# Performance work log

Hardware: AMD Instinct MI355X
Metric: run time of the kernel (lower is better)

The kernel has to match this reference:

```python
import jax, jax.numpy as jnp
import numpy as np

B_SZ, SEQ, D_MODEL, D_STATE, EXPAND = 2, 1024, 1024, 16, 2
D_INNER = D_MODEL * EXPAND


def setup_inputs() -> dict:
    key = jax.random.key(0)
    ks = jax.random.split(key, 11)
    f32 = jnp.float32
    x = jax.random.normal(ks[0], (B_SZ, SEQ, D_MODEL), f32)
    # nn.Linear-style params (weight stored as [out, in], applied as x @ W.T + b)
    s_in = 1.0 / np.sqrt(D_MODEL)
    W_in = jax.random.uniform(ks[1], (2 * D_INNER, D_MODEL), f32, -s_in, s_in)
    b_in = jax.random.uniform(ks[2], (2 * D_INNER,), f32, -s_in, s_in)
    W_gate = jax.random.uniform(ks[3], (D_INNER, D_MODEL), f32, -s_in, s_in)
    b_gate = jax.random.uniform(ks[4], (D_INNER,), f32, -s_in, s_in)
    s_out = 1.0 / np.sqrt(D_INNER)
    W_out = jax.random.uniform(ks[5], (D_MODEL, D_INNER), f32, -s_out, s_out)
    b_out = jax.random.uniform(ks[6], (D_MODEL,), f32, -s_out, s_out)
    A_log = jax.random.uniform(ks[7], (D_INNER, D_STATE), f32, -3.0, -1.0)
    B_mat = 0.02 * jax.random.normal(ks[8], (D_INNER, D_STATE), f32)
    C_mat = 0.02 * jax.random.normal(ks[9], (D_INNER, D_STATE), f32)
    D_vec = 0.02 * jax.random.normal(ks[10], (D_INNER,), f32)
    return {"x": x, "W_in": W_in, "b_in": b_in, "W_gate": W_gate,
            "b_gate": b_gate, "W_out": W_out, "b_out": b_out,
            "A_log": A_log, "B_mat": B_mat, "C_mat": C_mat, "D_vec": D_vec}


def _selective_scan(x, delta, A_log, B_mat, C_mat, D_vec):
    # x, delta: [B, S, d_inner]
    A = -jnp.exp(A_log)            # [d_inner, d_state]
    c0 = C_mat[0]                  # [d_state]; torch code's [:,0,:,0] reads only C row 0

    def step(h, inp):
        x_t, d_t = inp             # each [B, d_inner]
        h = h * jnp.exp(A * d_t[..., None]) + (x_t * d_t)[..., None] * B_mat
        y_t = h @ c0               # [B, d_inner]
        return h, y_t

    h0 = jnp.zeros((x.shape[0], A.shape[0], A.shape[1]), x.dtype)
    xs = (jnp.moveaxis(x, 1, 0), jnp.moveaxis(delta, 1, 0))  # time-major
    _, ys = jax.lax.scan(step, h0, xs)                       # ys: [S, B, d_inner]
    y = jnp.moveaxis(ys, 0, 1)
    return y + x * D_vec


def reference(x, W_in, b_in, W_gate, b_gate, W_out, b_out, A_log, B_mat, C_mat, D_vec):
    gate = jax.nn.sigmoid(x @ W_gate.T + b_gate)            # [B,S,d_inner]
    proj = x @ W_in.T + b_in                                # [B,S,2*d_inner]
    x_proj, delta_proj = jnp.split(proj, 2, axis=-1)
    delta = jax.nn.relu(delta_proj)
    ss = _selective_scan(x_proj, delta, A_log, B_mat, C_mat, D_vec)
    return (gate * ss) @ W_out.T + b_out                    # [B,S,d_model]
```

## Files before the change

kernel.cpp:

```cpp
#include <hip/hip_runtime.h>
#include <hip/hip_bf16.h>


#define LOG2E 1.4426950408889634f

typedef float floatx4 __attribute__((ext_vector_type(4)));
typedef short short8 __attribute__((ext_vector_type(8)));

__device__ __forceinline__ float fexp2(float x) { return __builtin_amdgcn_exp2f(x); }
__device__ __forceinline__ unsigned short f2bf(float f) {
    unsigned int u = __float_as_uint(f);
    u = (u + 0x7fffu + ((u >> 16) & 1u)) >> 16;
    return (unsigned short)u;
}
__device__ __forceinline__ float bf2f(unsigned short h) {
    return __uint_as_float(((unsigned int)h) << 16);
}

#define GLDS16(gp, lp) __builtin_amdgcn_global_load_lds(                      \
    (const __attribute__((address_space(1))) void*)(gp),                      \
    (__attribute__((address_space(3))) void*)(lp), 16, 0, 0)

__global__ __launch_bounds__(256) void cast_to_bf16(
    const float* __restrict__ x, const float* __restrict__ wg,
    const float* __restrict__ wi, const float* __restrict__ wo,
    unsigned short* __restrict__ ox, unsigned short* __restrict__ owg,
    unsigned short* __restrict__ owi, unsigned short* __restrict__ owo)
{
    const size_t e = ((size_t)blockIdx.x * 256 + threadIdx.x) * 4;
    const float* src; unsigned short* dst; size_t off;
    if (e < 2097152)      { src = x;  dst = ox;  off = e; }
    else if (e < 4194304) { src = wg; dst = owg; off = e - 2097152; }
    else if (e < 8388608) { src = wi; dst = owi; off = e - 4194304; }
    else                  { src = wo; dst = owo; off = e - 8388608; }
    float4 v = *(const float4*)(src + off);
    *(ushort4*)(dst + off) = make_ushort4(f2bf(v.x), f2bf(v.y), f2bf(v.z), f2bf(v.w));
}

template <int MODE, int MI>
__global__ __launch_bounds__(256, 2) void gemm_mfma(
    const unsigned short* __restrict__ A,
    const unsigned short* __restrict__ W0,
    const unsigned short* __restrict__ W1,
    const float* __restrict__ bias0, const float* __restrict__ bias1,
    unsigned short* __restrict__ gate,
    float* __restrict__ xproj, float* __restrict__ delta,
    float* __restrict__ outp, int K)
{
    constexpr int BM = MI * 32;
    constexpr int ROWA = BM / 32;
    __shared__ short As[BM * 64];
    __shared__ short Bs[128 * 64];

    const int tid = threadIdx.x;
    const int l = tid & 63, w = tid >> 6;
    const int mbase = blockIdx.y * BM;

    const unsigned short* Wp; const float* bias; int nbase; bool isGate = false;
    if (MODE == 3) {
        const int bx = blockIdx.x;
        if (bx < 16) { Wp = W0; bias = bias0; nbase = bx * 128; isGate = true; }
        else         { Wp = W1; bias = bias1; nbase = (bx - 16) * 128; }
    } else { Wp = W0; bias = bias0; nbase = blockIdx.x * 128; }

    const int rl = l >> 3;
    const int cs = (l & 7) ^ rl;
    size_t aoff[ROWA], boff[4];
    #pragma unroll
    for (int j = 0; j < ROWA; ++j)
        aoff[j] = (size_t)(mbase + (w * ROWA + j) * 8 + rl) * K + cs * 8;
    #pragma unroll
    for (int j = 0; j < 4; ++j)
        boff[j] = (size_t)(nbase + (w * 4 + j) * 8 + rl) * K + cs * 8;

    const int wm = (w >> 1) * (MI * 16), wn = (w & 1) * 64;
    floatx4 acc[MI][4] = {};

    for (int k0 = 0; k0 < K; k0 += 64) {
        __syncthreads();
        #pragma unroll
        for (int j = 0; j < ROWA; ++j)
            GLDS16(A + aoff[j] + k0, &As[(w * ROWA + j) * 512]);
        #pragma unroll
        for (int j = 0; j < 4; ++j)
            GLDS16(Wp + boff[j] + k0, &Bs[(w * 4 + j) * 512]);
        __syncthreads();

        #pragma unroll
        for (int kk = 0; kk < 2; ++kk) {
            short8 af[MI], bfr[4];
            #pragma unroll
            for (int i = 0; i < MI; ++i) {
                const int row = wm + i * 16 + (l & 15);
                af[i] = *(const short8*)&As[row * 64 + (((kk * 4 + (l >> 4)) ^ (row & 7)) << 3)];
            }
            #pragma unroll
            for (int j = 0; j < 4; ++j) {
                const int row = wn + j * 16 + (l & 15);
                bfr[j] = *(const short8*)&Bs[row * 64 + (((kk * 4 + (l >> 4)) ^ (row & 7)) << 3)];
            }
            #pragma unroll
            for (int i = 0; i < MI; ++i)
                #pragma unroll
                for (int j = 0; j < 4; ++j)
                    acc[i][j] = __builtin_amdgcn_mfma_f32_16x16x32_bf16(af[i], bfr[j], acc[i][j], 0, 0, 0);
        }
    }

    const int crow0 = wm + (l >> 4) * 4;
    const int ccol = wn + (l & 15);
    #pragma unroll
    for (int j = 0; j < 4; ++j) {
        const int n = nbase + ccol + j * 16;
        const float bb = bias[n];
        #pragma unroll
        for (int i = 0; i < MI; ++i) {
            const int mr = mbase + crow0 + i * 16;
            #pragma unroll
            for (int r = 0; r < 4; ++r) {
                const float v = acc[i][j][r] + bb;
                const int m = mr + r;
                if (MODE == 3) {
                    if (isGate) {
                        const float s = 1.0f / (1.0f + fexp2(-v * LOG2E));
                        gate[(size_t)m * 2048 + n] = f2bf(s);
                    } else if (n < 2048) {
                        xproj[(size_t)m * 2048 + n] = v;
                    } else {
                        delta[(size_t)m * 2048 + (n - 2048)] = fmaxf(v, 0.0f);
                    }
                } else {
                    outp[(size_t)m * 1024 + n] = v;
                }
            }
        }
    }
}

constexpr int NC = 32, CL = 32;

__global__ __launch_bounds__(256) void scan_phaseA(
    const float* __restrict__ xp, const float* __restrict__ dl,
    const float* __restrict__ A_log, const float* __restrict__ B_mat,
    float* __restrict__ Q, float* __restrict__ sumdt)
{
    const int ch = blockIdx.x * 256 + threadIdx.x;
    const int c = blockIdx.y;
    const int d = ch & 2047, b = ch >> 11;
    float Ac[16], Bv[16], h[16];
    #pragma unroll
    for (int s = 0; s < 16; ++s) {
        Ac[s] = -fexp2(A_log[d * 16 + s] * LOG2E) * LOG2E;
        Bv[s] = B_mat[d * 16 + s];
        h[s] = 0.0f;
    }
    float sd = 0.0f;
    size_t idx = ((size_t)b * 1024 + (size_t)c * CL) * 2048 + d;
    for (int t = 0; t < CL; ++t, idx += 2048) {
        const float xt = xp[idx], dt = dl[idx];
        sd += dt;
        const float xdt = xt * dt;
        #pragma unroll
        for (int s = 0; s < 16; ++s)
            h[s] = fmaf(h[s], fexp2(Ac[s] * dt), xdt * Bv[s]);
    }
    float* q = Q + ((size_t)ch * NC + c) * 16;
    #pragma unroll
    for (int s = 0; s < 16; ++s) q[s] = h[s];
    sumdt[ch * NC + c] = sd;
}

__global__ __launch_bounds__(256) void scan_phaseB(
    const float* __restrict__ A_log, const float* __restrict__ Q,
    const float* __restrict__ sumdt, float* __restrict__ hst)
{
    const int s = threadIdx.x & 15;
    const int ch = blockIdx.x * 16 + (threadIdx.x >> 4);
    const int d = ch & 2047;
    const float Ac = -fexp2(A_log[d * 16 + s] * LOG2E) * LOG2E;
    float h = 0.0f;
    const float* q = Q + (size_t)ch * NC * 16 + s;
    const float* sd = sumdt + ch * NC;
    float* hs = hst + (size_t)ch * NC * 16 + s;
    for (int c = 0; c < NC; ++c) {
        hs[c * 16] = h;
        h = fmaf(h, fexp2(Ac * sd[c]), q[c * 16]);
    }
}

__global__ __launch_bounds__(256) void scan_phaseC(
    const float* __restrict__ xp, const float* __restrict__ dl,
    const float* __restrict__ A_log, const float* __restrict__ B_mat,
    const float* __restrict__ C_mat, const float* __restrict__ D_vec,
    const unsigned short* __restrict__ gate, const float* __restrict__ hst,
    unsigned short* __restrict__ z)
{
    const int ch = blockIdx.x * 256 + threadIdx.x;
    const int c = blockIdx.y;
    const int d = ch & 2047, b = ch >> 11;
    float Ac[16], Bv[16], Cv[16], h[16];
    #pragma unroll
    for (int s = 0; s < 16; ++s) {
        Ac[s] = -fexp2(A_log[d * 16 + s] * LOG2E) * LOG2E;
        Bv[s] = B_mat[d * 16 + s];
        Cv[s] = C_mat[s];
        h[s] = hst[((size_t)ch * NC + c) * 16 + s];
    }
    const float Dv = D_vec[d];
    size_t idx = ((size_t)b * 1024 + (size_t)c * CL) * 2048 + d;
    for (int t = 0; t < CL; ++t, idx += 2048) {
        const float xt = xp[idx], dt = dl[idx];
        const float xdt = xt * dt;
        float y = 0.0f;
        #pragma unroll
        for (int s = 0; s < 16; ++s) {
            h[s] = fmaf(h[s], fexp2(Ac[s] * dt), xdt * Bv[s]);
            y = fmaf(h[s], Cv[s], y);
        }
        const float g = bf2f(gate[idx]);
        z[idx] = f2bf(g * (y + xt * Dv));
    }
}

extern "C" void kernel_launch(void* const* d_in, const int* in_sizes, int n_in,
                              void* d_out, int out_size, void* d_ws, size_t ws_size,
                              hipStream_t stream) {
    const float* x      = (const float*)d_in[0];
    const float* W_in   = (const float*)d_in[1];
    const float* b_in   = (const float*)d_in[2];
    const float* W_gate = (const float*)d_in[3];
    const float* b_gate = (const float*)d_in[4];
    const float* W_out  = (const float*)d_in[5];
    const float* b_out  = (const float*)d_in[6];
    const float* A_log  = (const float*)d_in[7];
    const float* B_mat  = (const float*)d_in[8];
    const float* C_mat  = (const float*)d_in[9];
    const float* D_vec  = (const float*)d_in[10];
    float* out = (float*)d_out;

    float* fws = (float*)d_ws;
    float* xproj = fws;
    float* delta = xproj + 4194304;
    float* Q     = delta + 4194304;
    float* hst   = Q + 2097152;
    float* sumdt = hst + 2097152;
    unsigned short* us = (unsigned short*)(sumdt + 131072);
    unsigned short* gate  = us;
    unsigned short* z     = gate + 4194304;
    unsigned short* x_bf  = z + 4194304;
    unsigned short* wg_bf = x_bf + 2097152;
    unsigned short* wi_bf = wg_bf + 2097152;
    unsigned short* wo_bf = wi_bf + 4194304;

    dim3 blk(256);
    cast_to_bf16<<<10240, blk, 0, stream>>>(x, W_gate, W_in, W_out, x_bf, wg_bf, wi_bf, wo_bf);
    gemm_mfma<3, 4><<<dim3(48, 16), blk, 0, stream>>>(
        x_bf, wg_bf, wi_bf, b_gate, b_in, gate, xproj, delta, nullptr, 1024);
    scan_phaseA<<<dim3(16, NC), blk, 0, stream>>>(xproj, delta, A_log, B_mat, Q, sumdt);
    scan_phaseB<<<256, blk, 0, stream>>>(A_log, Q, sumdt, hst);
    scan_phaseC<<<dim3(16, NC), blk, 0, stream>>>(xproj, delta, A_log, B_mat, C_mat, D_vec, gate, hst, z);
    gemm_mfma<2, 2><<<dim3(8, 32), blk, 0, stream>>>(
        z, wo_bf, nullptr, b_out, nullptr, nullptr, nullptr, nullptr, out, 2048);
}
```

Measured before the change: 209.6 us.

## Store xproj/delta in bf16, split-K out GEMM with atomics, raise occupancy

The fused input GEMM now writes xproj and delta as bf16 instead of fp32, which halves the bytes the scan phases read and write. The output GEMM uses split-K over two z-slices and accumulates with float atomicAdd into an output pre-filled with the bias by a new kernel, so the grid has more blocks. Launch bounds are raised to 3 blocks per CU. The cost is lower precision on the scan inputs, an extra kernel launch, and atomic contention plus non-deterministic summation order.

```diff
diff --git a/kernel.cpp b/kernel.cpp
--- a/kernel.cpp
+++ b/kernel.cpp
@@ -37,15 +37,23 @@
     *(ushort4*)(dst + off) = make_ushort4(f2bf(v.x), f2bf(v.y), f2bf(v.z), f2bf(v.w));
 }
 
+__global__ __launch_bounds__(256) void bias_init(
+    const float* __restrict__ bias, float* __restrict__ out)
+{
+    const size_t e = ((size_t)blockIdx.x * 256 + threadIdx.x) * 4;
+    const int col = (int)(e & 1023);
+    *(float4*)(out + e) = *(const float4*)(bias + col);
+}
+
 template <int MODE, int MI>
-__global__ __launch_bounds__(256, 2) void gemm_mfma(
+__global__ __launch_bounds__(256, 3) void gemm_mfma(
     const unsigned short* __restrict__ A,
     const unsigned short* __restrict__ W0,
     const unsigned short* __restrict__ W1,
     const float* __restrict__ bias0, const float* __restrict__ bias1,
     unsigned short* __restrict__ gate,
-    float* __restrict__ xproj, float* __restrict__ delta,
-    float* __restrict__ outp, int K)
+    unsigned short* __restrict__ xproj, unsigned short* __restrict__ delta,
+    float* __restrict__ outp, int ldk, int Ksub)
 {
     constexpr int BM = MI * 32;
     constexpr int ROWA = BM / 32;
@@ -55,28 +63,30 @@
     const int tid = threadIdx.x;
     const int l = tid & 63, w = tid >> 6;
     const int mbase = blockIdx.y * BM;
-
-    const unsigned short* Wp; const float* bias; int nbase; bool isGate = false;
+    const int kbeg = (MODE == 2) ? blockIdx.z * Ksub : 0;
+    const int kend = kbeg + Ksub;
+
+    const unsigned short* Wp; const float* bias = nullptr; int nbase; bool isGate = false;
     if (MODE == 3) {
         const int bx = blockIdx.x;
         if (bx < 16) { Wp = W0; bias = bias0; nbase = bx * 128; isGate = true; }
         else         { Wp = W1; bias = bias1; nbase = (bx - 16) * 128; }
-    } else { Wp = W0; bias = bias0; nbase = blockIdx.x * 128; }
+    } else { Wp = W0; nbase = blockIdx.x * 128; }
 
     const int rl = l >> 3;
     const int cs = (l & 7) ^ rl;
     size_t aoff[ROWA], boff[4];
     #pragma unroll
     for (int j = 0; j < ROWA; ++j)
-        aoff[j] = (size_t)(mbase + (w * ROWA + j) * 8 + rl) * K + cs * 8;
+        aoff[j] = (size_t)(mbase + (w * ROWA + j) * 8 + rl) * ldk + cs * 8;
     #pragma unroll
     for (int j = 0; j < 4; ++j)
-        boff[j] = (size_t)(nbase + (w * 4 + j) * 8 + rl) * K + cs * 8;
+        boff[j] = (size_t)(nbase + (w * 4 + j) * 8 + rl) * ldk + cs * 8;
 
     const int wm = (w >> 1) * (MI * 16), wn = (w & 1) * 64;
     floatx4 acc[MI][4] = {};
 
-    for (int k0 = 0; k0 < K; k0 += 64) {
+    for (int k0 = kbeg; k0 < kend; k0 += 64) {
         __syncthreads();
         #pragma unroll
         for (int j = 0; j < ROWA; ++j)
@@ -112,7 +122,7 @@
     #pragma unroll
     for (int j = 0; j < 4; ++j) {
         const int n = nbase + ccol + j * 16;
-        const float bb = bias[n];
+        const float bb = (MODE == 2) ? 0.0f : bias[n];
         #pragma unroll
         for (int i = 0; i < MI; ++i) {
             const int mr = mbase + crow0 + i * 16;
@@ -125,12 +135,12 @@
                         const float s = 1.0f / (1.0f + fexp2(-v * LOG2E));
                         gate[(size_t)m * 2048 + n] = f2bf(s);
                     } else if (n < 2048) {
-                        xproj[(size_t)m * 2048 + n] = v;
+                        xproj[(size_t)m * 2048 + n] = f2bf(v);
                     } else {
-                        delta[(size_t)m * 2048 + (n - 2048)] = fmaxf(v, 0.0f);
+                        delta[(size_t)m * 2048 + (n - 2048)] = f2bf(fmaxf(v, 0.0f));
                     }
                 } else {
-                    outp[(size_t)m * 1024 + n] = v;
+                    atomicAdd(&outp[(size_t)m * 1024 + n], v);
                 }
             }
         }
@@ -140,7 +150,7 @@
 constexpr int NC = 32, CL = 32;
 
 __global__ __launch_bounds__(256) void scan_phaseA(
-    const float* __restrict__ xp, const float* __restrict__ dl,
+    const unsigned short* __restrict__ xp, const unsigned short* __restrict__ dl,
     const float* __restrict__ A_log, const float* __restrict__ B_mat,
     float* __restrict__ Q, float* __restrict__ sumdt)
 {
@@ -157,7 +167,7 @@
     float sd = 0.0f;
     size_t idx = ((size_t)b * 1024 + (size_t)c * CL) * 2048 + d;
     for (int t = 0; t < CL; ++t, idx += 2048) {
-        const float xt = xp[idx], dt = dl[idx];
+        const float xt = bf2f(xp[idx]), dt = bf2f(dl[idx]);
         sd += dt;
         const float xdt = xt * dt;
         #pragma unroll
@@ -189,7 +199,7 @@
 }
 
 __global__ __launch_bounds__(256) void scan_phaseC(
-    const float* __restrict__ xp, const float* __restrict__ dl,
+    const unsigned short* __restrict__ xp, const unsigned short* __restrict__ dl,
     const float* __restrict__ A_log, const float* __restrict__ B_mat,
     const float* __restrict__ C_mat, const float* __restrict__ D_vec,
     const unsigned short* __restrict__ gate, const float* __restrict__ hst,
@@ -209,7 +219,7 @@
     const float Dv = D_vec[d];
     size_t idx = ((size_t)b * 1024 + (size_t)c * CL) * 2048 + d;
     for (int t = 0; t < CL; ++t, idx += 2048) {
-        const float xt = xp[idx], dt = dl[idx];
+        const float xt = bf2f(xp[idx]), dt = bf2f(dl[idx]);
         const float xdt = xt * dt;
         float y = 0.0f;
         #pragma unroll
@@ -238,27 +248,28 @@
     const float* D_vec  = (const float*)d_in[10];
     float* out = (float*)d_out;
 
-    float* fws = (float*)d_ws;
-    float* xproj = fws;
-    float* delta = xproj + 4194304;
-    float* Q     = delta + 4194304;
+    unsigned short* us = (unsigned short*)d_ws;
+    unsigned short* gate  = us;
+    unsigned short* z     = gate  + 4194304;
+    unsigned short* x_bf  = z     + 4194304;
+    unsigned short* wg_bf = x_bf  + 2097152;
+    unsigned short* wi_bf = wg_bf + 2097152;
+    unsigned short* wo_bf = wi_bf + 4194304;
+    unsigned short* xproj = wo_bf + 2097152;
+    unsigned short* delta = xproj + 4194304;
+    float* fws = (float*)(delta + 4194304);
+    float* Q     = fws;
     float* hst   = Q + 2097152;
     float* sumdt = hst + 2097152;
-    unsigned short* us = (unsigned short*)(sumdt + 131072);
-    unsigned short* gate  = us;
-    unsigned short* z     = gate + 4194304;
-    unsigned short* x_bf  = z + 4194304;
-    unsigned short* wg_bf = x_bf + 2097152;
-    unsigned short* wi_bf = wg_bf + 2097152;
-    unsigned short* wo_bf = wi_bf + 4194304;
 
     dim3 blk(256);
     cast_to_bf16<<<10240, blk, 0, stream>>>(x, W_gate, W_in, W_out, x_bf, wg_bf, wi_bf, wo_bf);
     gemm_mfma<3, 4><<<dim3(48, 16), blk, 0, stream>>>(
-        x_bf, wg_bf, wi_bf, b_gate, b_in, gate, xproj, delta, nullptr, 1024);
+        x_bf, wg_bf, wi_bf, b_gate, b_in, gate, xproj, delta, nullptr, 1024, 1024);
     scan_phaseA<<<dim3(16, NC), blk, 0, stream>>>(xproj, delta, A_log, B_mat, Q, sumdt);
     scan_phaseB<<<256, blk, 0, stream>>>(A_log, Q, sumdt, hst);
     scan_phaseC<<<dim3(16, NC), blk, 0, stream>>>(xproj, delta, A_log, B_mat, C_mat, D_vec, gate, hst, z);
-    gemm_mfma<2, 2><<<dim3(8, 32), blk, 0, stream>>>(
-        z, wo_bf, nullptr, b_out, nullptr, nullptr, nullptr, nullptr, out, 2048);
-}
+    bias_init<<<2048, blk, 0, stream>>>(b_out, out);
+    gemm_mfma<2, 2><<<dim3(8, 32, 2), blk, 0, stream>>>(
+        z, wo_bf, nullptr, nullptr, nullptr, nullptr, nullptr, nullptr, out, 2048, 1024);
+}
```

New measurement: 214.8 us. 2.5% more time.
